# Performance work log

Measured on AMD Instinct MI355X. Metric: run time of the kernel, lower is better.

## Reference

```python
import jax, jax.numpy as jnp
import numpy as np

N, NV, NE, NH = 256, 2048, 64, 4


def setup_inputs() -> dict:
    key = jax.random.key(0)
    ks = jax.random.split(key, 8)
    vertices = jax.random.normal(ks[0], (N, NV, NE), dtype=jnp.float32)
    mask = (jax.random.uniform(ks[1], (N, NV)) < 0.9).astype(jnp.float32)
    # learned input-independent query, init uniform(-init_w, init_w)
    query = jax.random.uniform(ks[2], (NE,), minval=-0.003, maxval=0.003, dtype=jnp.float32)
    # fc_createheads: Linear(NE -> NH*NE)
    Wc = jax.random.normal(ks[3], (NH * NE, NE), dtype=jnp.float32) / np.sqrt(NE).astype(np.float32)
    bc = jnp.zeros((NH * NE,), dtype=jnp.float32)
    # fc_logit: Linear(NE -> 1)
    wl = jax.random.normal(ks[4], (NE,), dtype=jnp.float32) / np.sqrt(NE).astype(np.float32)
    bl = jnp.zeros((), dtype=jnp.float32)
    # fc_reduceheads: Linear(NH*NE -> NE)
    Wr = jax.random.normal(ks[5], (NE, NH * NE), dtype=jnp.float32) / np.sqrt(NH * NE).astype(np.float32)
    br = jnp.zeros((NE,), dtype=jnp.float32)
    # learned softmax temperature (scalar Parameter, init 1.0)
    temp = jnp.asarray(1.0, dtype=jnp.float32)
    return dict(vertices=vertices, mask=mask, query=query, Wc=Wc, bc=bc,
                wl=wl, bl=bl, Wr=Wr, br=br, temp=temp)


def reference(vertices, mask, query, Wc, bc, wl, bl, Wr, br, temp):
    # query: learned (NE,) -> heads via fc_createheads -> (NH, NE); nQ == 1
    qh = (Wc @ query + bc).reshape(NH, NE)
    # additive attention logits: fc_logit(tanh(context + query)) -> (N, nV, nH)
    logits = jnp.tanh(vertices[:, :, None, :] + qh) @ wl + bl
    m = mask[:, :, None]  # (N, nV, 1)
    masked_logits = logits / temp * m - 99999.0 * (1.0 - m)
    probs = jax.nn.softmax(masked_logits, axis=1)  # softmax over nV
    # masked weighted sum of memory: (N, nH, nE)
    heads = jnp.einsum('nvh,nve,nv->nhe', probs, vertices, mask)
    heads = jax.nn.leaky_relu(heads, 0.01)  # F.leaky_relu default slope
    out = heads.reshape(vertices.shape[0], NH * NE) @ Wr.T + br  # (N, NE)
    return out[:, None, :]  # (N, 1, NE) to match torch (N, nQ, nE)
```

## Files before the change

### kernel.cpp

```cpp
#include <hip/hip_runtime.h>
#include <math.h>

namespace {
constexpr int NN = 256;
constexpr int NV = 2048;
constexpr int NE = 64;
constexpr int NH = 4;
}

typedef float vf4 __attribute__((ext_vector_type(4)));

template<int CTRL>
__device__ __forceinline__ float dpp_add(float x) {
    const int xi = __float_as_int(x);
    const int yi = __builtin_amdgcn_update_dpp(0, xi, CTRL, 0xF, 0xF, true);
    return x + __int_as_float(yi);
}
__device__ __forceinline__ float row16_sum(float x) {
    x = dpp_add<0xB1>(x);
    x = dpp_add<0x4E>(x);
    x = dpp_add<0x141>(x);
    x = dpp_add<0x140>(x);
    return x;
}

__global__ void qh_kernel(const float* __restrict__ Wc,
                          const float* __restrict__ query,
                          const float* __restrict__ bc,
                          float* __restrict__ qh) {
    const int i = threadIdx.x;
    float acc = bc[i];
    #pragma unroll
    for (int k = 0; k < NE; k += 4) {
        const float4 w = *reinterpret_cast<const float4*>(Wc + i * NE + k);
        const float4 q = *reinterpret_cast<const float4*>(query + k);
        acc += w.x * q.x + w.y * q.y + w.z * q.z + w.w * q.w;
    }
    qh[i] = acc;
}

template<int CHUNKS>
__global__ __launch_bounds__(256, 4) void pool1_kernel(
    const float* __restrict__ vertices,
    const float* __restrict__ mask,
    const float* __restrict__ qh,
    const float* __restrict__ wl,
    const float* __restrict__ blp,
    const float* __restrict__ tempp,
    float* __restrict__ partN,
    float* __restrict__ partZ)
{
    constexpr int ROWS_B = NV / CHUNKS;
    constexpr int ROWS_W = ROWS_B / 4;
    constexpr int ITERS  = ROWS_W / 4;

    __shared__ float sp[4][NH][NE];
    __shared__ float sz[4][NH];

    const int tid   = threadIdx.x;
    const int lane  = tid & 63;
    const int wid   = tid >> 6;
    const int n     = blockIdx.x / CHUNKS;
    const int chunk = blockIdx.x % CHUNKS;
    const int eq    = (lane & 15) * 4;
    const int rg    = lane >> 4;

    const vf4 wlf = *reinterpret_cast<const vf4*>(wl + eq);
    const float wls[4] = {wlf.x, wlf.y, wlf.z, wlf.w};
    float A[NH][4];
    #pragma unroll
    for (int h = 0; h < NH; ++h) {
        const vf4 q = *reinterpret_cast<const vf4*>(qh + h * NE + eq);
        A[h][0] = wls[0] * q.x; A[h][1] = wls[1] * q.y;
        A[h][2] = wls[2] * q.z; A[h][3] = wls[3] * q.w;
    }
    const float bl    = blp[0];
    const float rtemp = 1.0f / tempp[0];

    float nacc[NH][4] = {};
    float zacc[NH]    = {};

    const float* vb = vertices + (size_t)n * NV * NE;
    const float* mb = mask + (size_t)n * NV;
    const int rbase = chunk * ROWS_B + wid * ROWS_W;

    #pragma unroll 4
    for (int it = 0; it < ITERS; ++it) {
        const int row = rbase + it * 4 + rg;
        const vf4   x = *reinterpret_cast<const vf4*>(vb + (size_t)row * NE + eq);
        const float m = mb[row];
        const float xs[4] = {x.x, x.y, x.z, x.w};

        float u[4], s0 = 0.f;
        #pragma unroll
        for (int j = 0; j < 4; ++j) {
            const float ez = __expf(xs[j] + xs[j]);
            const float r  = __builtin_amdgcn_rcpf(ez + 1.0f);
            const float t  = __builtin_fmaf(-2.0f, r, 1.0f);
            u[j] = __builtin_fmaf(-t, t, 1.0f);
            s0   = __builtin_fmaf(wls[j], t, s0);
        }
        float s[NH];
        #pragma unroll
        for (int h = 0; h < NH; ++h) {
            float sh = s0;
            #pragma unroll
            for (int j = 0; j < 4; ++j)
                sh = __builtin_fmaf(A[h][j], u[j], sh);
            s[h] = row16_sum(sh);
        }
        const float rm = rtemp * m;
        const float c  = __builtin_fmaf(bl, rm,
                           __builtin_fmaf(99999.0f, m, -99999.0f));
        #pragma unroll
        for (int h = 0; h < NH; ++h) {
            const float w = __expf(__builtin_fmaf(s[h], rm, c));
            zacc[h] += w;
            #pragma unroll
            for (int j = 0; j < 4; ++j)
                nacc[h][j] = __builtin_fmaf(w, xs[j], nacc[h][j]);
        }
    }

    #pragma unroll
    for (int off = 16; off <= 32; off <<= 1) {
        #pragma unroll
        for (int h = 0; h < NH; ++h) {
            #pragma unroll
            for (int j = 0; j < 4; ++j)
                nacc[h][j] += __shfl_xor(nacc[h][j], off, 64);
            zacc[h] += __shfl_xor(zacc[h], off, 64);
        }
    }

    if (rg == 0) {
        #pragma unroll
        for (int h = 0; h < NH; ++h) {
            sp[wid][h][eq + 0] = nacc[h][0];
            sp[wid][h][eq + 1] = nacc[h][1];
            sp[wid][h][eq + 2] = nacc[h][2];
            sp[wid][h][eq + 3] = nacc[h][3];
        }
        if (lane == 0) {
            #pragma unroll
            for (int h = 0; h < NH; ++h) sz[wid][h] = zacc[h];
        }
    }
    __syncthreads();
    {
        const int h = tid >> 6, e = tid & 63;
        const float v = sp[0][h][e] + sp[1][h][e] + sp[2][h][e] + sp[3][h][e];
        partN[(((size_t)n * CHUNKS + chunk) * NH + h) * NE + e] = v;
    }
    if (tid < NH) {
        const float z = sz[0][tid] + sz[1][tid] + sz[2][tid] + sz[3][tid];
        partZ[((size_t)n * CHUNKS + chunk) * NH + tid] = z;
    }
}

__global__ __launch_bounds__(256) void pool2_kernel(
    int chunks,
    const float* __restrict__ partN,
    const float* __restrict__ partZ,
    const float* __restrict__ Wr,
    const float* __restrict__ br,
    float* __restrict__ out)
{
    __shared__ float heads[NH * NE];
    const int n = blockIdx.x, tid = threadIdx.x;
    const int h = tid >> 6, e = tid & 63;

    float num = 0.f, Z = 0.f;
    for (int c = 0; c < chunks; ++c) {
        num += partN[(((size_t)n * chunks + c) * NH + h) * NE + e];
        Z   += partZ[((size_t)n * chunks + c) * NH + h];
    }
    const float val = num / Z;
    heads[tid] = (val > 0.f) ? val : 0.01f * val;
    __syncthreads();

    {
        const int eo = tid >> 2;
        const int ko = (tid & 3) * 64;
        float acc = 0.f;
        #pragma unroll
        for (int k = 0; k < 64; k += 4) {
            const float4 w = *reinterpret_cast<const float4*>(Wr + eo * (NH * NE) + ko + k);
            acc += heads[ko + k + 0] * w.x + heads[ko + k + 1] * w.y +
                   heads[ko + k + 2] * w.z + heads[ko + k + 3] * w.w;
        }
        acc += __shfl_xor(acc, 1, 64);
        acc += __shfl_xor(acc, 2, 64);
        if ((tid & 3) == 0) out[(size_t)n * NE + eo] = acc + br[eo];
    }
}

extern "C" void kernel_launch(void* const* d_in, const int* in_sizes, int n_in,
                              void* d_out, int out_size, void* d_ws, size_t ws_size,
                              hipStream_t stream) {
    const float* vertices = (const float*)d_in[0];
    const float* mask     = (const float*)d_in[1];
    const float* query    = (const float*)d_in[2];
    const float* Wc       = (const float*)d_in[3];
    const float* bc       = (const float*)d_in[4];
    const float* wl       = (const float*)d_in[5];
    const float* bl       = (const float*)d_in[6];
    const float* Wr       = (const float*)d_in[7];
    const float* br       = (const float*)d_in[8];
    const float* temp     = (const float*)d_in[9];
    float* out = (float*)d_out;

    auto need = [](int chunks) -> size_t {
        return (size_t)(256 + NN * chunks * NH + (size_t)NN * chunks * NH * NE) * 4;
    };
    int chunks = 8;
    while (chunks > 1 && need(chunks) > ws_size) chunks >>= 1;

    float* qh    = (float*)d_ws;
    float* partZ = qh + 256;
    float* partN = partZ + (size_t)NN * chunks * NH;

    qh_kernel<<<1, 256, 0, stream>>>(Wc, query, bc, qh);
    switch (chunks) {
        case 8:  pool1_kernel<8><<<NN * 8, 256, 0, stream>>>(vertices, mask, qh, wl, bl, temp, partN, partZ); break;
        case 4:  pool1_kernel<4><<<NN * 4, 256, 0, stream>>>(vertices, mask, qh, wl, bl, temp, partN, partZ); break;
        case 2:  pool1_kernel<2><<<NN * 2, 256, 0, stream>>>(vertices, mask, qh, wl, bl, temp, partN, partZ); break;
        default: pool1_kernel<1><<<NN * 1, 256, 0, stream>>>(vertices, mask, qh, wl, bl, temp, partN, partZ); break;
    }
    pool2_kernel<<<NN, 256, 0, stream>>>(chunks, partN, partZ, Wr, br, out);
}
```

Measured before the change: 42.47 us.

## Double-buffer vertex tiles into LDS via global_load_lds async copies

Replaces direct per-thread global loads of vertex rows with a double-buffered LDS pipeline. Each 64-row tile is copied with global_load_lds while the previous tile is computed from shared memory, and the mask chunk is staged in LDS as well. The goal is to overlap memory latency with the tanh/exp compute. In exchange it adds a barrier per tile and about 32KB+ of LDS per block, which can cut occupancy below the launch-bounds target, and it drops the workspace-size fallback by hardcoding chunks=8. The wait before the first barrier depends on the compiler inserting vmcnt waits for the LDS-DMA loads, which is a correctness risk.

```diff
diff --git a/kernel.cpp b/kernel.cpp
--- a/kernel.cpp
+++ b/kernel.cpp
@@ -22,6 +22,13 @@
     x = dpp_add<0x141>(x);
     x = dpp_add<0x140>(x);
     return x;
+}
+
+__device__ __forceinline__ void stage16(const float* g, float* l) {
+    typedef unsigned int u32;
+    auto gp = (const __attribute__((address_space(1))) u32*)g;
+    auto lp = (__attribute__((address_space(3))) u32*)l;
+    __builtin_amdgcn_global_load_lds(gp, lp, 16, 0, 0);
 }
 
 __global__ void qh_kernel(const float* __restrict__ Wc,
@@ -51,9 +58,12 @@
     float* __restrict__ partZ)
 {
     constexpr int ROWS_B = NV / CHUNKS;
-    constexpr int ROWS_W = ROWS_B / 4;
-    constexpr int ITERS  = ROWS_W / 4;
-
+    constexpr int TILE   = 64;
+    constexpr int NT     = ROWS_B / TILE;
+    constexpr int LPW    = TILE * NE / (4 * 64 * 4);
+
+    __shared__ float buf[2][TILE * NE];
+    __shared__ float mask_s[ROWS_B];
     __shared__ float sp[4][NH][NE];
     __shared__ float sz[4][NH];
 
@@ -80,45 +90,63 @@
     float nacc[NH][4] = {};
     float zacc[NH]    = {};
 
-    const float* vb = vertices + (size_t)n * NV * NE;
-    const float* mb = mask + (size_t)n * NV;
-    const int rbase = chunk * ROWS_B + wid * ROWS_W;
-
-    #pragma unroll 4
-    for (int it = 0; it < ITERS; ++it) {
-        const int row = rbase + it * 4 + rg;
-        const vf4   x = *reinterpret_cast<const vf4*>(vb + (size_t)row * NE + eq);
-        const float m = mb[row];
-        const float xs[4] = {x.x, x.y, x.z, x.w};
-
-        float u[4], s0 = 0.f;
-        #pragma unroll
-        for (int j = 0; j < 4; ++j) {
-            const float ez = __expf(xs[j] + xs[j]);
-            const float r  = __builtin_amdgcn_rcpf(ez + 1.0f);
-            const float t  = __builtin_fmaf(-2.0f, r, 1.0f);
-            u[j] = __builtin_fmaf(-t, t, 1.0f);
-            s0   = __builtin_fmaf(wls[j], t, s0);
-        }
-        float s[NH];
-        #pragma unroll
-        for (int h = 0; h < NH; ++h) {
-            float sh = s0;
-            #pragma unroll
-            for (int j = 0; j < 4; ++j)
-                sh = __builtin_fmaf(A[h][j], u[j], sh);
-            s[h] = row16_sum(sh);
-        }
-        const float rm = rtemp * m;
-        const float c  = __builtin_fmaf(bl, rm,
-                           __builtin_fmaf(99999.0f, m, -99999.0f));
-        #pragma unroll
-        for (int h = 0; h < NH; ++h) {
-            const float w = __expf(__builtin_fmaf(s[h], rm, c));
-            zacc[h] += w;
-            #pragma unroll
-            for (int j = 0; j < 4; ++j)
-                nacc[h][j] = __builtin_fmaf(w, xs[j], nacc[h][j]);
+    const int rblk = chunk * ROWS_B;
+    const float* vb = vertices + ((size_t)n * NV + rblk) * NE;
+    const float* mb = mask + (size_t)n * NV + rblk;
+
+    auto stage_tile = [&](int t) {
+        const float* g0 = vb + (size_t)t * TILE * NE;
+        #pragma unroll
+        for (int k = 0; k < LPW; ++k) {
+            const int off = (wid * LPW + k) * 256;
+            stage16(g0 + off + lane * 4, &buf[t & 1][off]);
+        }
+    };
+
+    mask_s[tid] = mb[tid];
+    stage_tile(0);
+
+    for (int t = 0; t < NT; ++t) {
+        __syncthreads();
+        if (t + 1 < NT) stage_tile(t + 1);
+
+        const float* bufc = buf[t & 1];
+        #pragma unroll
+        for (int it = 0; it < TILE / 16; ++it) {
+            const int r = wid * (TILE / 4) + it * 4 + rg;
+            const vf4   x = *reinterpret_cast<const vf4*>(&bufc[r * NE + eq]);
+            const float m = mask_s[t * TILE + r];
+            const float xs[4] = {x.x, x.y, x.z, x.w};
+
+            float u[4], s0 = 0.f;
+            #pragma unroll
+            for (int j = 0; j < 4; ++j) {
+                const float ez = __expf(xs[j] + xs[j]);
+                const float r_ = __builtin_amdgcn_rcpf(ez + 1.0f);
+                const float tt = __builtin_fmaf(-2.0f, r_, 1.0f);
+                u[j] = __builtin_fmaf(-tt, tt, 1.0f);
+                s0   = __builtin_fmaf(wls[j], tt, s0);
+            }
+            float s[NH];
+            #pragma unroll
+            for (int h = 0; h < NH; ++h) {
+                float sh = s0;
+                #pragma unroll
+                for (int j = 0; j < 4; ++j)
+                    sh = __builtin_fmaf(A[h][j], u[j], sh);
+                s[h] = row16_sum(sh);
+            }
+            const float rm = rtemp * m;
+            const float c  = __builtin_fmaf(bl, rm,
+                               __builtin_fmaf(99999.0f, m, -99999.0f));
+            #pragma unroll
+            for (int h = 0; h < NH; ++h) {
+                const float w = __expf(__builtin_fmaf(s[h], rm, c));
+                zacc[h] += w;
+                #pragma unroll
+                for (int j = 0; j < 4; ++j)
+                    nacc[h][j] = __builtin_fmaf(w, xs[j], nacc[h][j]);
+            }
         }
     }
 
@@ -210,22 +238,13 @@
     const float* temp     = (const float*)d_in[9];
     float* out = (float*)d_out;
 
-    auto need = [](int chunks) -> size_t {
-        return (size_t)(256 + NN * chunks * NH + (size_t)NN * chunks * NH * NE) * 4;
-    };
-    int chunks = 8;
-    while (chunks > 1 && need(chunks) > ws_size) chunks >>= 1;
+    constexpr int chunks = 8;
 
     float* qh    = (float*)d_ws;
     float* partZ = qh + 256;
     float* partN = partZ + (size_t)NN * chunks * NH;
 
     qh_kernel<<<1, 256, 0, stream>>>(Wc, query, bc, qh);
-    switch (chunks) {
-        case 8:  pool1_kernel<8><<<NN * 8, 256, 0, stream>>>(vertices, mask, qh, wl, bl, temp, partN, partZ); break;
-        case 4:  pool1_kernel<4><<<NN * 4, 256, 0, stream>>>(vertices, mask, qh, wl, bl, temp, partN, partZ); break;
-        case 2:  pool1_kernel<2><<<NN * 2, 256, 0, stream>>>(vertices, mask, qh, wl, bl, temp, partN, partZ); break;
-        default: pool1_kernel<1><<<NN * 1, 256, 0, stream>>>(vertices, mask, qh, wl, bl, temp, partN, partZ); break;
-    }
+    pool1_kernel<chunks><<<NN * chunks, 256, 0, stream>>>(vertices, mask, qh, wl, bl, temp, partN, partZ);
     pool2_kernel<<<NN, 256, 0, stream>>>(chunks, partN, partZ, Wr, br, out);
 }
```

New measurement: 46.47 us. 1.09x slower.
